# Kernel tuning notes

Measured on AMD Instinct MI355X. Metric: run time of the kernel, lower is better.

The kernel has to match this reference:

```python
import jax, jax.numpy as jnp
import numpy as np

H = 16       # num_attention_heads
D = 64       # head_dim
WIN = 256    # local attention window_size


def setup_inputs() -> dict:
    key = jax.random.key(0)
    ks = jax.random.split(key, 6)
    B, S, E = 2, 2048, 1024
    sc = 1.0 / np.sqrt(E)
    return {
        "hidden_states": jax.random.normal(ks[0], (B, S, E), jnp.float32),
        "Wq": jax.random.normal(ks[1], (E, E), jnp.float32) * sc,
        "Wk": jax.random.normal(ks[2], (E, E), jnp.float32) * sc,
        "Wv": jax.random.normal(ks[3], (E, E), jnp.float32) * sc,
        "Wo": jax.random.normal(ks[4], (E, E), jnp.float32) * sc,
        "bo": jnp.zeros((E,), jnp.float32),
    }


def reference(hidden_states, Wq, Wk, Wv, Wo, bo):
    B, S, E = hidden_states.shape
    # torch Linear: y = x @ W^T
    q = (hidden_states @ Wq.T).reshape(B, S, H, D).transpose(0, 2, 1, 3)  # [B,H,S,D]
    k = (hidden_states @ Wk.T).reshape(B, S, H, D).transpose(0, 2, 1, 3)
    v = (hidden_states @ Wv.T).reshape(B, S, H, D).transpose(0, 2, 1, 3)

    # Eager path: fp32 QK^T, NO 1/sqrt(d) scaling (faithful to source)
    scores = jnp.einsum("bhqd,bhkd->bhqk", q.astype(jnp.float32), k.astype(jnp.float32))

    i = jnp.arange(S)[:, None]
    j = jnp.arange(S)[None, :]
    band = (j <= i) & (j > i - WIN)  # [S,S]
    mask_value = jnp.finfo(scores.dtype).min
    scores = jnp.where(band[None, None], scores, mask_value)

    attn = jax.nn.softmax(scores, axis=-1).astype(v.dtype)  # dropout p=0 -> identity
    ctx = jnp.einsum("bhqk,bhkd->bhqd", attn, v)              # [B,H,S,D]
    ctx = ctx.transpose(0, 2, 1, 3).reshape(B, S, E)          # merge heads
    return ctx @ Wo.T + bo
```

## Files before the change

### kernel.cpp

```cpp
#include <hip/hip_runtime.h>


typedef __bf16 bf16x8 __attribute__((ext_vector_type(8)));
typedef short s16x8 __attribute__((ext_vector_type(8)));
typedef float f32x4 __attribute__((ext_vector_type(4)));
typedef unsigned short u16;
typedef unsigned long long u64;

#define DEV __device__ __forceinline__

DEV u16 f2bf(float f) {
  unsigned u = __builtin_bit_cast(unsigned, f);
  u += 0x7FFFu + ((u >> 16) & 1u);
  return (u16)(u >> 16);
}
DEV float bf2f(u16 h) {
  unsigned u = ((unsigned)h) << 16;
  return __builtin_bit_cast(float, u);
}

#define MFMA16(a, b, c) __builtin_amdgcn_mfma_f32_16x16x32_bf16((a), (b), (c), 0, 0, 0)

DEV void gload16(const u16* g, u16* l) {
  __builtin_amdgcn_global_load_lds(
      (const __attribute__((address_space(1))) void*)(const void*)g,
      (__attribute__((address_space(3))) void*)(void*)l, 16, 0, 0);
}

DEV void stage_tile(const u16* __restrict__ g, size_t stride, int r0, int k0,
                    u16* lds, int w, int lane) {
#pragma unroll
  for (int c = 0; c < 2; ++c) {
    int ch = c * 256 + (w << 6) + lane;
    gload16(&g[(size_t)(r0 + (ch >> 2)) * stride + k0 + ((ch & 3) << 3)],
            lds + (size_t)(c * 4 + w) * 512);
  }
}

__global__ __launch_bounds__(256) void cvt_all(
    const float* __restrict__ x, const float* __restrict__ Wq,
    const float* __restrict__ Wk, const float* __restrict__ Wv,
    const float* __restrict__ Wo, u16* __restrict__ xh, u16* __restrict__ xl,
    u16* __restrict__ wh, u16* __restrict__ wl, u16* __restrict__ woh) {
  for (int i = blockIdx.x * 256 + threadIdx.x; i < 2097152;
       i += gridDim.x * 256) {
    const float* src;
    u16 *dh, *dl = nullptr;
    int off;
    bool sp;
    if (i < 1048576) {
      src = x; off = i; dh = xh; dl = xl; sp = true;
    } else {
      int j = i - 1048576;
      int r = j >> 18;
      off = j & 262143;
      if (r == 0)      { src = Wq; dh = wh;           dl = wl;           sp = true; }
      else if (r == 1) { src = Wk; dh = wh + 1048576; dl = wl + 1048576; sp = true; }
      else if (r == 2) { src = Wv; dh = wh + 2097152; sp = false; }
      else             { src = Wo; dh = woh;          sp = false; }
    }
    f32x4 v = ((const f32x4*)src)[off];
    u64 ph = 0, pl = 0;
#pragma unroll
    for (int c = 0; c < 4; ++c) {
      u16 h = f2bf(v[c]);
      ph |= ((u64)h) << (16 * c);
      u16 l = f2bf(v[c] - bf2f(h));
      pl |= ((u64)l) << (16 * c);
    }
    ((u64*)dh)[off] = ph;
    if (sp) ((u64*)dl)[off] = pl;
  }
}

__global__ __launch_bounds__(256, 3) void qkv_gemm(
    const u16* __restrict__ Xh, const u16* __restrict__ Xl,
    const u16* __restrict__ Wh, const u16* __restrict__ Wl,
    u16* __restrict__ qh, u16* __restrict__ ql, u16* __restrict__ kh,
    u16* __restrict__ kl, u16* __restrict__ vT) {
  __shared__ u16 sAh[128 * 32], sAl[128 * 32];
  __shared__ u16 sBh[128 * 32], sBl[128 * 32];
  const int tid = threadIdx.x, lane = tid & 63, w = tid >> 6;
  const int lr = lane & 15, lg = lane >> 4;
  const int wr = w >> 1, wc = w & 1;
  const int m0 = blockIdx.y * 128, n0 = blockIdx.x * 128;
  const int region = n0 >> 10;
  const bool split = region < 2;

  f32x4 acc[4][4];
#pragma unroll
  for (int i = 0; i < 4; ++i)
#pragma unroll
    for (int j = 0; j < 4; ++j)
#pragma unroll
      for (int e = 0; e < 4; ++e) acc[i][j][e] = 0.f;

  for (int k0 = 0; k0 < 1024; k0 += 32) {
    stage_tile(Xh, 1024, m0, k0, sAh, w, lane);
    stage_tile(Wh, 1024, n0, k0, sBh, w, lane);
    if (split) {
      stage_tile(Xl, 1024, m0, k0, sAl, w, lane);
      stage_tile(Wl, 1024, n0, k0, sBl, w, lane);
    }
    __syncthreads();

    bf16x8 fah[4], fbh[4], fal[4], fbl[4];
#pragma unroll
    for (int f = 0; f < 4; ++f) {
      fah[f] = *(const bf16x8*)&sAh[(wr * 64 + f * 16 + lr) * 32 + lg * 8];
      fbh[f] = *(const bf16x8*)&sBh[(wc * 64 + f * 16 + lr) * 32 + lg * 8];
    }
    if (split) {
#pragma unroll
      for (int f = 0; f < 4; ++f) {
        fal[f] = *(const bf16x8*)&sAl[(wr * 64 + f * 16 + lr) * 32 + lg * 8];
        fbl[f] = *(const bf16x8*)&sBl[(wc * 64 + f * 16 + lr) * 32 + lg * 8];
      }
#pragma unroll
      for (int i = 0; i < 4; ++i)
#pragma unroll
        for (int j = 0; j < 4; ++j) {
          acc[i][j] = MFMA16(fah[i], fbh[j], acc[i][j]);
          acc[i][j] = MFMA16(fah[i], fbl[j], acc[i][j]);
          acc[i][j] = MFMA16(fal[i], fbh[j], acc[i][j]);
        }
    } else {
#pragma unroll
      for (int i = 0; i < 4; ++i)
#pragma unroll
        for (int j = 0; j < 4; ++j)
          acc[i][j] = MFMA16(fah[i], fbh[j], acc[i][j]);
    }
    __syncthreads();
  }

#pragma unroll
  for (int i = 0; i < 4; ++i)
#pragma unroll
    for (int j = 0; j < 4; ++j)
#pragma unroll
      for (int e = 0; e < 4; ++e) {
        float v = acc[i][j][e];
        int mm = m0 + wr * 64 + i * 16 + lg * 4 + e;
        int nl = (n0 & 1023) + wc * 64 + j * 16 + lr;
        int bb = mm >> 11, ss = mm & 2047, hh = nl >> 6, dd = nl & 63;
        if (region == 0) {
          size_t idx = ((size_t)(bb * 16 + hh) * 2048 + ss) * 64 + dd;
          u16 h = f2bf(v);
          qh[idx] = h;
          ql[idx] = f2bf(v - bf2f(h));
        } else if (region == 1) {
          size_t idx = ((size_t)(bb * 16 + hh) * 2048 + ss) * 64 + dd;
          u16 h = f2bf(v);
          kh[idx] = h;
          kl[idx] = f2bf(v - bf2f(h));
        } else {
          vT[((size_t)(bb * 16 + hh) * 64 + dd) * 2048 + ss] = f2bf(v);
        }
      }
}

__global__ __launch_bounds__(256) void out_gemm(const u16* __restrict__ ctx,
                                                const u16* __restrict__ Wo,
                                                const float* __restrict__ bias,
                                                float* __restrict__ Of) {
  __shared__ u16 sA[128 * 32], sB[128 * 32];
  const int tid = threadIdx.x, lane = tid & 63, w = tid >> 6;
  const int lr = lane & 15, lg = lane >> 4;
  const int wr = w >> 1, wc = w & 1;
  const int m0 = blockIdx.y * 128, n0 = blockIdx.x * 128;

  f32x4 acc[4][4];
#pragma unroll
  for (int i = 0; i < 4; ++i)
#pragma unroll
    for (int j = 0; j < 4; ++j)
#pragma unroll
      for (int e = 0; e < 4; ++e) acc[i][j][e] = 0.f;

  for (int k0 = 0; k0 < 1024; k0 += 32) {
    stage_tile(ctx, 1024, m0, k0, sA, w, lane);
    stage_tile(Wo, 1024, n0, k0, sB, w, lane);
    __syncthreads();
    bf16x8 fa[4], fb[4];
#pragma unroll
    for (int f = 0; f < 4; ++f) {
      fa[f] = *(const bf16x8*)&sA[(wr * 64 + f * 16 + lr) * 32 + lg * 8];
      fb[f] = *(const bf16x8*)&sB[(wc * 64 + f * 16 + lr) * 32 + lg * 8];
    }
#pragma unroll
    for (int i = 0; i < 4; ++i)
#pragma unroll
      for (int j = 0; j < 4; ++j) acc[i][j] = MFMA16(fa[i], fb[j], acc[i][j]);
    __syncthreads();
  }
#pragma unroll
  for (int i = 0; i < 4; ++i)
#pragma unroll
    for (int j = 0; j < 4; ++j)
#pragma unroll
      for (int e = 0; e < 4; ++e) {
        int mm = m0 + wr * 64 + i * 16 + lg * 4 + e;
        int nn = n0 + wc * 64 + j * 16 + lr;
        Of[(size_t)mm * 1024 + nn] = acc[i][j][e] + bias[nn];
      }
}

__global__ __launch_bounds__(256) void attn_kernel(
    const u16* __restrict__ qh, const u16* __restrict__ ql,
    const u16* __restrict__ kh, const u16* __restrict__ kl,
    const u16* __restrict__ vT, u16* __restrict__ ctx) {
  const int qt = blockIdx.x, hd = blockIdx.y, b = blockIdx.z;
  const int q0 = qt * 64;
  const int bh = b * 16 + hd;
  const int tid = threadIdx.x;
  const int lane = tid & 63, w = tid >> 6;
  const int lr = lane & 15, lg = lane >> 4;

  __shared__ u16 sKh[64][72];
  __shared__ u16 sKl[64][72];
  __shared__ u16 sVT[64][72];
  __shared__ u16 sP[4][16][72];

  bf16x8 qfh[2], qfl[2];
  const size_t qbase = ((size_t)bh * 2048 + q0 + w * 16 + lr) * 64;
#pragma unroll
  for (int ks = 0; ks < 2; ++ks) {
    qfh[ks] = *(const bf16x8*)&qh[qbase + ks * 32 + lg * 8];
    qfl[ks] = *(const bf16x8*)&ql[qbase + ks * 32 + lg * 8];
  }

  float mrow[4], lrow[4];
  f32x4 cf[4];
#pragma unroll
  for (int e = 0; e < 4; ++e) { mrow[e] = -__builtin_inff(); lrow[e] = 0.f; }
#pragma unroll
  for (int nd = 0; nd < 4; ++nd)
#pragma unroll
    for (int e = 0; e < 4; ++e) cf[nd][e] = 0.f;

  const int t0 = (qt >= 4) ? qt - 4 : 0;
  for (int t = t0; t <= qt; ++t) {
    const int k0 = t * 64;
#pragma unroll
    for (int c = 0; c < 2; ++c) {
      int cid = c * 256 + tid;
      int row = cid >> 3, col8 = (cid & 7) * 8;
      size_t kidx = ((size_t)bh * 2048 + k0 + row) * 64 + col8;
      size_t vidx = ((size_t)bh * 64 + row) * 2048 + k0 + col8;
      *(s16x8*)&sKh[row][col8] = *(const s16x8*)&kh[kidx];
      *(s16x8*)&sKl[row][col8] = *(const s16x8*)&kl[kidx];
      *(s16x8*)&sVT[row][col8] = *(const s16x8*)&vT[vidx];
    }
    __syncthreads();

    f32x4 sc[4];
#pragma unroll
    for (int nf = 0; nf < 4; ++nf)
#pragma unroll
      for (int e = 0; e < 4; ++e) sc[nf][e] = 0.f;
#pragma unroll
    for (int ks = 0; ks < 2; ++ks)
#pragma unroll
      for (int nf = 0; nf < 4; ++nf) {
        bf16x8 kbh = *(const bf16x8*)&sKh[nf * 16 + lr][ks * 32 + lg * 8];
        bf16x8 kbl = *(const bf16x8*)&sKl[nf * 16 + lr][ks * 32 + lg * 8];
        sc[nf] = MFMA16(qfh[ks], kbh, sc[nf]);
        sc[nf] = MFMA16(qfh[ks], kbl, sc[nf]);
        sc[nf] = MFMA16(qfl[ks], kbh, sc[nf]);
      }

    const bool masked = (k0 < q0 - 192) || (k0 >= q0);
    if (masked) {
#pragma unroll
      for (int nf = 0; nf < 4; ++nf) {
        int key = k0 + nf * 16 + lr;
#pragma unroll
        for (int e = 0; e < 4; ++e) {
          int qi = q0 + w * 16 + lg * 4 + e;
          if (key > qi || key + 256 <= qi) sc[nf][e] = -__builtin_inff();
        }
      }
    }

    float rm[4];
#pragma unroll
    for (int e = 0; e < 4; ++e)
      rm[e] = fmaxf(fmaxf(sc[0][e], sc[1][e]), fmaxf(sc[2][e], sc[3][e]));
#pragma unroll
    for (int off = 1; off < 16; off <<= 1)
#pragma unroll
      for (int e = 0; e < 4; ++e) rm[e] = fmaxf(rm[e], __shfl_xor(rm[e], off));

    float alpha[4], mu[4];
#pragma unroll
    for (int e = 0; e < 4; ++e) {
      float mn = fmaxf(mrow[e], rm[e]);
      bool ninf = (mn == -__builtin_inff());
      mu[e] = ninf ? 0.f : mn;
      alpha[e] = ninf ? 1.f : __expf(mrow[e] - mn);
      mrow[e] = mn;
    }
    float p[4][4], rs[4];
#pragma unroll
    for (int nf = 0; nf < 4; ++nf)
#pragma unroll
      for (int e = 0; e < 4; ++e) p[nf][e] = __expf(sc[nf][e] - mu[e]);
#pragma unroll
    for (int e = 0; e < 4; ++e) rs[e] = p[0][e] + p[1][e] + p[2][e] + p[3][e];
#pragma unroll
    for (int off = 1; off < 16; off <<= 1)
#pragma unroll
      for (int e = 0; e < 4; ++e) rs[e] += __shfl_xor(rs[e], off);
#pragma unroll
    for (int e = 0; e < 4; ++e) lrow[e] = lrow[e] * alpha[e] + rs[e];
#pragma unroll
    for (int nd = 0; nd < 4; ++nd)
#pragma unroll
      for (int e = 0; e < 4; ++e) cf[nd][e] *= alpha[e];

#pragma unroll
    for (int nf = 0; nf < 4; ++nf)
#pragma unroll
      for (int e = 0; e < 4; ++e)
        sP[w][lg * 4 + e][nf * 16 + lr] = f2bf(p[nf][e]);

#pragma unroll
    for (int ks = 0; ks < 2; ++ks) {
      bf16x8 pa = *(const bf16x8*)&sP[w][lr][ks * 32 + lg * 8];
#pragma unroll
      for (int nd = 0; nd < 4; ++nd) {
        bf16x8 vb = *(const bf16x8*)&sVT[nd * 16 + lr][ks * 32 + lg * 8];
        cf[nd] = MFMA16(pa, vb, cf[nd]);
      }
    }
    __syncthreads();
  }

#pragma unroll
  for (int nd = 0; nd < 4; ++nd)
#pragma unroll
    for (int e = 0; e < 4; ++e) {
      float v = cf[nd][e] / lrow[e];
      size_t o = ((size_t)(b * 2048 + q0 + w * 16 + lg * 4 + e)) * 1024 +
                 hd * 64 + nd * 16 + lr;
      ctx[o] = f2bf(v);
    }
}

extern "C" void kernel_launch(void* const* d_in, const int* in_sizes, int n_in,
                              void* d_out, int out_size, void* d_ws, size_t ws_size,
                              hipStream_t stream) {
  (void)in_sizes; (void)n_in; (void)out_size; (void)ws_size;
  const float* x  = (const float*)d_in[0];
  const float* Wq = (const float*)d_in[1];
  const float* Wk = (const float*)d_in[2];
  const float* Wv = (const float*)d_in[3];
  const float* Wo = (const float*)d_in[4];
  const float* bo = (const float*)d_in[5];
  float* out = (float*)d_out;
  char* ws = (char*)d_ws;

  constexpr size_t MB = 1048576;
  u16* xh  = (u16*)(ws + 0 * MB);
  u16* xl  = (u16*)(ws + 8 * MB);
  u16* qh  = (u16*)(ws + 16 * MB);
  u16* ql  = (u16*)(ws + 24 * MB);
  u16* kh  = (u16*)(ws + 32 * MB);
  u16* kl  = (u16*)(ws + 40 * MB);
  u16* vT  = (u16*)(ws + 48 * MB);
  u16* ctx = (u16*)(ws + 56 * MB);
  u16* wh  = (u16*)(ws + 64 * MB);
  u16* wl  = (u16*)(ws + 70 * MB);
  u16* woh = (u16*)(ws + 74 * MB);

  cvt_all<<<2048, 256, 0, stream>>>(x, Wq, Wk, Wv, Wo, xh, xl, wh, wl, woh);
  qkv_gemm<<<dim3(24, 32), 256, 0, stream>>>(xh, xl, wh, wl, qh, ql, kh, kl, vT);
  attn_kernel<<<dim3(32, 16, 2), 256, 0, stream>>>(qh, ql, kh, kl, vT, ctx);
  out_gemm<<<dim3(8, 32), 256, 0, stream>>>(ctx, woh, bo, out);
}
```

Before: 309.1 us.

## Store V row-major and transpose in LDS, remap QKV blocks, shrink out_gemm tile

The QKV GEMM now writes V in the same [B,H,S,D] layout as Q and K, replacing the strided transposed scatter. The attention kernel transposes V while loading it into shared memory instead. The QKV grid is flattened and remapped so blocks are spread across XCDs. The output GEMM switches to 64x128 tiles, doubling the block count for better occupancy. The trade-offs are LDS bank conflicts from the scalar transposed stores and lower per-block reuse in the output GEMM.

```diff
diff --git a/kernel.cpp b/kernel.cpp
--- a/kernel.cpp
+++ b/kernel.cpp
@@ -77,13 +77,15 @@
     const u16* __restrict__ Xh, const u16* __restrict__ Xl,
     const u16* __restrict__ Wh, const u16* __restrict__ Wl,
     u16* __restrict__ qh, u16* __restrict__ ql, u16* __restrict__ kh,
-    u16* __restrict__ kl, u16* __restrict__ vT) {
+    u16* __restrict__ kl, u16* __restrict__ vh) {
   __shared__ u16 sAh[128 * 32], sAl[128 * 32];
   __shared__ u16 sBh[128 * 32], sBl[128 * 32];
   const int tid = threadIdx.x, lane = tid & 63, w = tid >> 6;
   const int lr = lane & 15, lg = lane >> 4;
   const int wr = w >> 1, wc = w & 1;
-  const int m0 = blockIdx.y * 128, n0 = blockIdx.x * 128;
+  const int bid = blockIdx.x;
+  const int flat = (bid & 7) * 96 + (bid >> 3);
+  const int m0 = (flat & 31) * 128, n0 = (flat >> 5) * 128;
   const int region = n0 >> 10;
   const bool split = region < 2;
 
@@ -144,64 +146,67 @@
         int mm = m0 + wr * 64 + i * 16 + lg * 4 + e;
         int nl = (n0 & 1023) + wc * 64 + j * 16 + lr;
         int bb = mm >> 11, ss = mm & 2047, hh = nl >> 6, dd = nl & 63;
+        size_t idx = ((size_t)(bb * 16 + hh) * 2048 + ss) * 64 + dd;
         if (region == 0) {
-          size_t idx = ((size_t)(bb * 16 + hh) * 2048 + ss) * 64 + dd;
           u16 h = f2bf(v);
           qh[idx] = h;
           ql[idx] = f2bf(v - bf2f(h));
         } else if (region == 1) {
-          size_t idx = ((size_t)(bb * 16 + hh) * 2048 + ss) * 64 + dd;
           u16 h = f2bf(v);
           kh[idx] = h;
           kl[idx] = f2bf(v - bf2f(h));
         } else {
-          vT[((size_t)(bb * 16 + hh) * 64 + dd) * 2048 + ss] = f2bf(v);
+          vh[idx] = f2bf(v);
         }
       }
 }
 
-__global__ __launch_bounds__(256) void out_gemm(const u16* __restrict__ ctx,
-                                                const u16* __restrict__ Wo,
-                                                const float* __restrict__ bias,
-                                                float* __restrict__ Of) {
-  __shared__ u16 sA[128 * 32], sB[128 * 32];
+__global__ __launch_bounds__(256, 2) void out_gemm(const u16* __restrict__ ctx,
+                                                   const u16* __restrict__ Wo,
+                                                   const float* __restrict__ bias,
+                                                   float* __restrict__ Of) {
+  __shared__ u16 sA[64 * 32], sB[128 * 32];
   const int tid = threadIdx.x, lane = tid & 63, w = tid >> 6;
   const int lr = lane & 15, lg = lane >> 4;
-  const int wr = w >> 1, wc = w & 1;
-  const int m0 = blockIdx.y * 128, n0 = blockIdx.x * 128;
-
-  f32x4 acc[4][4];
+  const int m0 = blockIdx.y * 64, n0 = blockIdx.x * 128;
+
+  f32x4 acc[4][2];
 #pragma unroll
   for (int i = 0; i < 4; ++i)
 #pragma unroll
-    for (int j = 0; j < 4; ++j)
+    for (int j = 0; j < 2; ++j)
 #pragma unroll
       for (int e = 0; e < 4; ++e) acc[i][j][e] = 0.f;
 
   for (int k0 = 0; k0 < 1024; k0 += 32) {
-    stage_tile(ctx, 1024, m0, k0, sA, w, lane);
+    {
+      int ch = (w << 6) + lane;
+      gload16(&ctx[(size_t)(m0 + (ch >> 2)) * 1024 + k0 + ((ch & 3) << 3)],
+              sA + (size_t)w * 512);
+    }
     stage_tile(Wo, 1024, n0, k0, sB, w, lane);
     __syncthreads();
-    bf16x8 fa[4], fb[4];
-#pragma unroll
-    for (int f = 0; f < 4; ++f) {
-      fa[f] = *(const bf16x8*)&sA[(wr * 64 + f * 16 + lr) * 32 + lg * 8];
-      fb[f] = *(const bf16x8*)&sB[(wc * 64 + f * 16 + lr) * 32 + lg * 8];
-    }
+    bf16x8 fa[4], fb[2];
+#pragma unroll
+    for (int f = 0; f < 4; ++f)
+      fa[f] = *(const bf16x8*)&sA[(f * 16 + lr) * 32 + lg * 8];
+#pragma unroll
+    for (int j = 0; j < 2; ++j)
+      fb[j] = *(const bf16x8*)&sB[(w * 32 + j * 16 + lr) * 32 + lg * 8];
 #pragma unroll
     for (int i = 0; i < 4; ++i)
 #pragma unroll
-      for (int j = 0; j < 4; ++j) acc[i][j] = MFMA16(fa[i], fb[j], acc[i][j]);
+      for (int j = 0; j < 2; ++j) acc[i][j] = MFMA16(fa[i], fb[j], acc[i][j]);
     __syncthreads();
   }
 #pragma unroll
   for (int i = 0; i < 4; ++i)
 #pragma unroll
-    for (int j = 0; j < 4; ++j)
+    for (int j = 0; j < 2; ++j)
 #pragma unroll
       for (int e = 0; e < 4; ++e) {
-        int mm = m0 + wr * 64 + i * 16 + lg * 4 + e;
-        int nn = n0 + wc * 64 + j * 16 + lr;
+        int mm = m0 + i * 16 + lg * 4 + e;
+        int nn = n0 + w * 32 + j * 16 + lr;
         Of[(size_t)mm * 1024 + nn] = acc[i][j][e] + bias[nn];
       }
 }
@@ -209,7 +214,7 @@
 __global__ __launch_bounds__(256) void attn_kernel(
     const u16* __restrict__ qh, const u16* __restrict__ ql,
     const u16* __restrict__ kh, const u16* __restrict__ kl,
-    const u16* __restrict__ vT, u16* __restrict__ ctx) {
+    const u16* __restrict__ vh, u16* __restrict__ ctx) {
   const int qt = blockIdx.x, hd = blockIdx.y, b = blockIdx.z;
   const int q0 = qt * 64;
   const int bh = b * 16 + hd;
@@ -247,10 +252,12 @@
       int cid = c * 256 + tid;
       int row = cid >> 3, col8 = (cid & 7) * 8;
       size_t kidx = ((size_t)bh * 2048 + k0 + row) * 64 + col8;
-      size_t vidx = ((size_t)bh * 64 + row) * 2048 + k0 + col8;
       *(s16x8*)&sKh[row][col8] = *(const s16x8*)&kh[kidx];
       *(s16x8*)&sKl[row][col8] = *(const s16x8*)&kl[kidx];
-      *(s16x8*)&sVT[row][col8] = *(const s16x8*)&vT[vidx];
+      s16x8 vv = *(const s16x8*)&vh[kidx];
+#pragma unroll
+      for (int j = 0; j < 8; ++j)
+        sVT[col8 + j][row] = (u16)vv[j];
     }
     __syncthreads();
 
@@ -368,14 +375,14 @@
   u16* ql  = (u16*)(ws + 24 * MB);
   u16* kh  = (u16*)(ws + 32 * MB);
   u16* kl  = (u16*)(ws + 40 * MB);
-  u16* vT  = (u16*)(ws + 48 * MB);
+  u16* vh  = (u16*)(ws + 48 * MB);
   u16* ctx = (u16*)(ws + 56 * MB);
   u16* wh  = (u16*)(ws + 64 * MB);
   u16* wl  = (u16*)(ws + 70 * MB);
   u16* woh = (u16*)(ws + 74 * MB);
 
   cvt_all<<<2048, 256, 0, stream>>>(x, Wq, Wk, Wv, Wo, xh, xl, wh, wl, woh);
-  qkv_gemm<<<dim3(24, 32), 256, 0, stream>>>(xh, xl, wh, wl, qh, ql, kh, kl, vT);
-  attn_kernel<<<dim3(32, 16, 2), 256, 0, stream>>>(qh, ql, kh, kl, vT, ctx);
-  out_gemm<<<dim3(8, 32), 256, 0, stream>>>(ctx, woh, bo, out);
-}
+  qkv_gemm<<<768, 256, 0, stream>>>(xh, xl, wh, wl, qh, ql, kh, kl, vh);
+  attn_kernel<<<dim3(32, 16, 2), 256, 0, stream>>>(qh, ql, kh, kl, vh, ctx);
+  out_gemm<<<dim3(8, 64), 256, 0, stream>>>(ctx, woh, bo, out);
+}
```

Result: slower. 327.4 us (+5.9%).
